# Performance work log

Hardware: AMD Instinct MI355X
Metric: run time of the kernel (lower is better)

Reference implementation:

```python
import jax, jax.numpy as jnp
import numpy as np

THRESHOLD = 33.33  # torch forward default

def setup_inputs() -> dict:
    key = jax.random.key(0)
    k1, k2 = jax.random.split(key)
    source_pc = jax.random.normal(k1, (2, 16384, 3), dtype=jnp.float32)
    target_pc = jax.random.normal(k2, (2, 16384, 3), dtype=jnp.float32)
    return {"source_pc": source_pc, "target_pc": target_pc}

def _pairwise_dist(x, y):
    # Euclidean cdist via the matmul expansion (same math as torch.cdist p=2).
    # x: [B, N, D], y: [B, M, D] -> [B, N, M]
    x2 = jnp.sum(x * x, axis=-1)              # [B, N]
    y2 = jnp.sum(y * y, axis=-1)              # [B, M]
    xy = jnp.einsum('bnd,bmd->bnm', x, y)     # [B, N, M]
    d2 = x2[:, :, None] + y2[None if False else slice(None), None, :] - 2.0 * xy
    d2 = x2[:, :, None] + y2[:, None, :] - 2.0 * xy
    return jnp.sqrt(jnp.maximum(d2, 0.0))

def reference(source_pc, target_pc):
    dist = _pairwise_dist(source_pc.astype(jnp.float32), target_pc.astype(jnp.float32))
    dist1 = jnp.minimum(jnp.min(dist, axis=2), THRESHOLD)  # [B, N] clamped
    dist2 = jnp.minimum(jnp.min(dist, axis=1), THRESHOLD)  # [B, M] clamped
    d1 = jnp.mean(dist1, axis=-1)
    d2 = jnp.mean(dist2, axis=-1)
    return (d1 + d2) / 2.0  # bidirectional=True default -> [B]
```

## Files before the change

### kernel.cpp

```cpp
#include <hip/hip_runtime.h>

#define NPTS 16384
#define TH 33.33f

typedef __attribute__((ext_vector_type(8)))  __bf16 bf16x8;
typedef __attribute__((ext_vector_type(16))) float  f32x16;

__device__ __forceinline__ unsigned short f2bf(float x) {
    unsigned u = __float_as_uint(x);
    u += 0x7FFFu + ((u >> 16) & 1u);
    return (unsigned short)(u >> 16);
}
__device__ __forceinline__ float bf2f(unsigned short h) {
    return __uint_as_float(((unsigned)h) << 16);
}

union UV { uint4 v; bf16x8 h; unsigned short s[8]; };


#define FOLD1(MM, AA, QQ) { \
    f32x16 t = __builtin_amdgcn_mfma_f32_32x32x16_bf16(AA, QQ, zc, 0, 0, 0); \
    _Pragma("unroll") for (int j = 0; j < 16; j++) MM[j] = fmaxf(MM[j], t[j]); }

__device__ __forceinline__ void conv_store(unsigned short* lb, int k,
                                           float x, float y, float z) {
    float hp = 0.5f * fmaf(z, z, fmaf(y, y, x * x));
    unsigned short xh = f2bf(x), yh = f2bf(y), zh = f2bf(z);
    unsigned short xl = f2bf(x - bf2f(xh)), yl = f2bf(y - bf2f(yh)), zl = f2bf(z - bf2f(zh));
    float rr = hp;
    unsigned short h0 = f2bf(rr); rr -= bf2f(h0);
    unsigned short h1 = f2bf(rr); rr -= bf2f(h1);
    unsigned short h2 = f2bf(rr);
    UV c0, c1;
    c0.s[0]=xh; c0.s[1]=yh; c0.s[2]=zh; c0.s[3]=xh; c0.s[4]=yh; c0.s[5]=zh; c0.s[6]=xl; c0.s[7]=yl;
    c1.s[0]=zl; c1.s[1]=(unsigned short)(h0^0x8000); c1.s[2]=(unsigned short)(h1^0x8000);
    c1.s[3]=(unsigned short)(h2^0x8000); c1.s[4]=0; c1.s[5]=0; c1.s[6]=0; c1.s[7]=0;
    int t = k >> 5, pos = k & 31;
    *(uint4*)(lb + t * 512 + pos * 8)       = c0.v;
    *(uint4*)(lb + t * 512 + 256 + pos * 8) = c1.v;
}

#define LOAD_PTS(CC) { \
    const float* gp_ = pp + (size_t)(seg * 2048 + (CC) * 512 + tid * 2) * 3; \
    pf0 = *(const float2*)(gp_ + 0); \
    pf1 = *(const float2*)(gp_ + 2); \
    pf2 = *(const float2*)(gp_ + 4); }

#define CONV_WRITE(BUF) { \
    unsigned short* lb = (unsigned short*)(smem + (BUF) * 16384); \
    conv_store(lb, tid * 2,     pf0.x, pf0.y, pf1.x); \
    conv_store(lb, tid * 2 + 1, pf1.y, pf2.x, pf2.y); }

#define EPILOG(MM, P) { \
    float* sc = scratch + wave * 1056; \
    _Pragma("unroll") for (int j = 0; j < 16; j++) { \
        int r0 = (j & 3) + 8 * (j >> 2) + 4 * g; sc[r0 * 33 + cc] = MM[j]; } \
    __syncthreads(); \
    const float* sr = sc + cc * 33 + g * 16; \
    float mx = -3.0e38f; \
    _Pragma("unroll") for (int k = 0; k < 16; k++) mx = fmaxf(mx, sr[k]); \
    mx = fmaxf(mx, __shfl_xor(mx, 32, 64)); \
    if (lane < 32) { \
        float d2 = 2.0f * (hq[P] - mx); \
        float d = fminf(sqrtf(fmaxf(d2, 0.0f)), TH); \
        dst[wave * 64 + (P) * 32 + lane] = d; } \
    __syncthreads(); }

__global__ __launch_bounds__(256, 4) void chamfer_kernel(
        const float* __restrict__ src, const float* __restrict__ tgt,
        float* __restrict__ d2part)
{
    const int db = blockIdx.y, dir = db >> 1, b = db & 1;
    const int rowblock = blockIdx.x >> 3, seg = blockIdx.x & 7;
    const int tid = threadIdx.x, wave = tid >> 6, lane = tid & 63;
    const int g = lane >> 5, cc = lane & 31;
    const float* qp = (dir == 0 ? src : tgt) + (size_t)b * NPTS * 3;
    const float* pp = (dir == 0 ? tgt : src) + (size_t)b * NPTS * 3;
    const unsigned short one = 0x3F80;

    __shared__ alignas(16) unsigned char smem[32768];
    float* scratch = (float*)smem;

    const int rt0 = rowblock * 8 + wave * 2;
    bf16x8 afrag[2]; float hq[2];
#pragma unroll
    for (int i = 0; i < 2; i++) {
        int r = (rt0 + i) * 32 + cc;
        float x = qp[r * 3 + 0], y = qp[r * 3 + 1], z = qp[r * 3 + 2];
        hq[i] = 0.5f * fmaf(z, z, fmaf(y, y, x * x));
        unsigned short xh = f2bf(x), yh = f2bf(y), zh = f2bf(z);
        unsigned short xl = f2bf(x - bf2f(xh)), yl = f2bf(y - bf2f(yh)), zl = f2bf(z - bf2f(zh));
        UV f0, f1, rv;
        f0.s[0]=xh; f0.s[1]=yh; f0.s[2]=zh; f0.s[3]=xl; f0.s[4]=yl; f0.s[5]=zl; f0.s[6]=xh; f0.s[7]=yh;
        f1.s[0]=zh; f1.s[1]=one; f1.s[2]=one; f1.s[3]=one; f1.s[4]=0; f1.s[5]=0; f1.s[6]=0; f1.s[7]=0;
        rv.v = g ? f1.v : f0.v;
        afrag[i] = rv.h;
    }

    f32x16 m0 = -3.0e38f, m1 = -3.0e38f;
    const f32x16 zc = 0.0f;
    float2 pf0, pf1, pf2;

    LOAD_PTS(0)
    CONV_WRITE(0)
    __syncthreads();
#pragma unroll 1
    for (int c = 0; c < 4; ++c) {
        if (c < 3) LOAD_PTS(c + 1)
        const unsigned short* bb = (const unsigned short*)(smem + (c & 1) * 16384);
#pragma unroll 1
        for (int pt = 0; pt < 8; ++pt) {
            bf16x8 q0 = *(const bf16x8*)(bb + pt * 1024 + lane * 8);
            FOLD1(m0, afrag[0], q0)
            FOLD1(m1, afrag[1], q0)
            bf16x8 q1 = *(const bf16x8*)(bb + pt * 1024 + 512 + lane * 8);
            FOLD1(m0, afrag[0], q1)
            FOLD1(m1, afrag[1], q1)
        }
        if (c < 3) CONV_WRITE((c + 1) & 1)
        __syncthreads();
    }

    float* dst = d2part + (((size_t)(db * 64 + rowblock)) * 8 + seg) * 256;
    EPILOG(m0, 0)
    EPILOG(m1, 1)
}

__global__ __launch_bounds__(256) void merge_kernel(const float* __restrict__ d2part,
                                                    float* __restrict__ out) {
    const int b = blockIdx.y;
    const int slice = blockIdx.x;
    const int tid = threadIdx.x;
    float s = 0.0f;
#pragma unroll
    for (int pass = 0; pass < 2; pass++) {
        const float* base = d2part + (size_t)(pass * 2 + b) * 64 * 8 * 256;
#pragma unroll
        for (int i = 0; i < 4; i++) {
            int r = slice * 1024 + i * 256 + tid;
            const float* p = base + (size_t)(r >> 8) * 2048 + (r & 255);
            float m = p[0];
#pragma unroll
            for (int sgi = 1; sgi < 8; sgi++) m = fminf(m, p[sgi * 256]);
            s += m;
        }
    }
#pragma unroll
    for (int off = 32; off > 0; off >>= 1) s += __shfl_down(s, off, 64);
    __shared__ float w[4];
    if ((tid & 63) == 0) w[tid >> 6] = s;
    __syncthreads();
    if (tid == 0) {
        float t = (w[0] + w[1]) + (w[2] + w[3]);
        atomicAdd(&out[b], t * (1.0f / (2.0f * NPTS)));
    }
}

extern "C" void kernel_launch(void* const* d_in, const int* in_sizes, int n_in,
                              void* d_out, int out_size, void* d_ws, size_t ws_size,
                              hipStream_t stream) {
    const float* src = (const float*)d_in[0];
    const float* tgt = (const float*)d_in[1];
    float* out = (float*)d_out;
    float* d2part = (float*)d_ws;

    hipMemsetAsync(out, 0, 2 * sizeof(float), stream);
    chamfer_kernel<<<dim3(512, 4), 256, 0, stream>>>(src, tgt, d2part);
    merge_kernel<<<dim3(16, 2), 256, 0, stream>>>(d2part, out);
}
```

Measured before the change: 96.77 us.

## Halve LDS staging, shuffle-based epilogue, fold output zeroing into kernel

The LDS staging buffer shrinks from 32 KB to 16 KB by moving to 8 chunks of 256 points, one point per thread. This lets launch bounds request 8 blocks per SM instead of 4. The epilogue now reduces the MFMA max accumulators with cross-lane shuffles instead of an LDS transpose and two block barriers. The output memset is dropped and the main kernel zeroes the output instead, which removes one launch. The trade-offs are twice as many barrier-separated chunks, possible register pressure under the higher occupancy target, and reliance on the chamfer kernel finishing before the merge kernel's atomic adds.

```diff
diff --git a/kernel.cpp b/kernel.cpp
--- a/kernel.cpp
+++ b/kernel.cpp
@@ -41,45 +41,41 @@
 }
 
 #define LOAD_PTS(CC) { \
-    const float* gp_ = pp + (size_t)(seg * 2048 + (CC) * 512 + tid * 2) * 3; \
-    pf0 = *(const float2*)(gp_ + 0); \
-    pf1 = *(const float2*)(gp_ + 2); \
-    pf2 = *(const float2*)(gp_ + 4); }
+    const float* g0 = pp + (size_t)(seg * 2048 + (CC) * 256 + tid) * 3; \
+    px = g0[0]; py = g0[1]; pz = g0[2]; }
 
 #define CONV_WRITE(BUF) { \
-    unsigned short* lb = (unsigned short*)(smem + (BUF) * 16384); \
-    conv_store(lb, tid * 2,     pf0.x, pf0.y, pf1.x); \
-    conv_store(lb, tid * 2 + 1, pf1.y, pf2.x, pf2.y); }
+    conv_store((unsigned short*)(smem + (BUF) * 8192), tid, px, py, pz); }
 
-#define EPILOG(MM, P) { \
-    float* sc = scratch + wave * 1056; \
+#define EPILOG(MM, HQ, OFF) { \
     _Pragma("unroll") for (int j = 0; j < 16; j++) { \
-        int r0 = (j & 3) + 8 * (j >> 2) + 4 * g; sc[r0 * 33 + cc] = MM[j]; } \
-    __syncthreads(); \
-    const float* sr = sc + cc * 33 + g * 16; \
-    float mx = -3.0e38f; \
-    _Pragma("unroll") for (int k = 0; k < 16; k++) mx = fmaxf(mx, sr[k]); \
-    mx = fmaxf(mx, __shfl_xor(mx, 32, 64)); \
-    if (lane < 32) { \
-        float d2 = 2.0f * (hq[P] - mx); \
-        float d = fminf(sqrtf(fmaxf(d2, 0.0f)), TH); \
-        dst[wave * 64 + (P) * 32 + lane] = d; } \
-    __syncthreads(); }
+        float red = MM[j]; \
+        red = fmaxf(red, __shfl_xor(red, 1, 64)); \
+        red = fmaxf(red, __shfl_xor(red, 2, 64)); \
+        red = fmaxf(red, __shfl_xor(red, 4, 64)); \
+        red = fmaxf(red, __shfl_xor(red, 8, 64)); \
+        red = fmaxf(red, __shfl_xor(red, 16, 64)); \
+        int r0 = (j & 3) + 8 * (j >> 2) + 4 * g; \
+        float hqr = __shfl(HQ, r0, 64); \
+        if (cc == j) { \
+            float d2 = 2.0f * (hqr - red); \
+            float d = fminf(sqrtf(fmaxf(d2, 0.0f)), TH); \
+            dst[wave * 64 + (OFF) + r0] = d; } } }
 
-__global__ __launch_bounds__(256, 4) void chamfer_kernel(
+__global__ __launch_bounds__(256, 8) void chamfer_kernel(
         const float* __restrict__ src, const float* __restrict__ tgt,
-        float* __restrict__ d2part)
+        float* __restrict__ d2part, float* __restrict__ out)
 {
     const int db = blockIdx.y, dir = db >> 1, b = db & 1;
     const int rowblock = blockIdx.x >> 3, seg = blockIdx.x & 7;
     const int tid = threadIdx.x, wave = tid >> 6, lane = tid & 63;
     const int g = lane >> 5, cc = lane & 31;
+    if (blockIdx.x == 0 && db == 0 && tid < 2) out[tid] = 0.0f;
     const float* qp = (dir == 0 ? src : tgt) + (size_t)b * NPTS * 3;
     const float* pp = (dir == 0 ? tgt : src) + (size_t)b * NPTS * 3;
     const unsigned short one = 0x3F80;
 
-    __shared__ alignas(16) unsigned char smem[32768];
-    float* scratch = (float*)smem;
+    __shared__ alignas(16) unsigned char smem[16384];
 
     const int rt0 = rowblock * 8 + wave * 2;
     bf16x8 afrag[2]; float hq[2];
@@ -99,17 +95,17 @@
 
     f32x16 m0 = -3.0e38f, m1 = -3.0e38f;
     const f32x16 zc = 0.0f;
-    float2 pf0, pf1, pf2;
+    float px, py, pz;
 
     LOAD_PTS(0)
     CONV_WRITE(0)
     __syncthreads();
 #pragma unroll 1
-    for (int c = 0; c < 4; ++c) {
-        if (c < 3) LOAD_PTS(c + 1)
-        const unsigned short* bb = (const unsigned short*)(smem + (c & 1) * 16384);
+    for (int c = 0; c < 8; ++c) {
+        if (c < 7) LOAD_PTS(c + 1)
+        const unsigned short* bb = (const unsigned short*)(smem + (c & 1) * 8192);
 #pragma unroll 1
-        for (int pt = 0; pt < 8; ++pt) {
+        for (int pt = 0; pt < 4; ++pt) {
             bf16x8 q0 = *(const bf16x8*)(bb + pt * 1024 + lane * 8);
             FOLD1(m0, afrag[0], q0)
             FOLD1(m1, afrag[1], q0)
@@ -117,13 +113,13 @@
             FOLD1(m0, afrag[0], q1)
             FOLD1(m1, afrag[1], q1)
         }
-        if (c < 3) CONV_WRITE((c + 1) & 1)
+        if (c < 7) CONV_WRITE((c + 1) & 1)
         __syncthreads();
     }
 
     float* dst = d2part + (((size_t)(db * 64 + rowblock)) * 8 + seg) * 256;
-    EPILOG(m0, 0)
-    EPILOG(m1, 1)
+    EPILOG(m0, hq[0], 0)
+    EPILOG(m1, hq[1], 32)
 }
 
 __global__ __launch_bounds__(256) void merge_kernel(const float* __restrict__ d2part,
@@ -164,7 +160,6 @@
     float* out = (float*)d_out;
     float* d2part = (float*)d_ws;
 
-    hipMemsetAsync(out, 0, 2 * sizeof(float), stream);
-    chamfer_kernel<<<dim3(512, 4), 256, 0, stream>>>(src, tgt, d2part);
+    chamfer_kernel<<<dim3(512, 4), 256, 0, stream>>>(src, tgt, d2part, out);
     merge_kernel<<<dim3(16, 2), 256, 0, stream>>>(d2part, out);
 }
```

Measured after the change: 309.0 us. +219.3%, slower.
